# Optimization experiments

Hardware: AMD Instinct MI355X
Metric: run time of the kernel (lower is better)

The kernel has to match this reference:

```python
import jax, jax.numpy as jnp
import numpy as np

# Original torch code does the CZT in float64/complex128 explicitly; match it.
jax.config.update("jax_enable_x64", True)

SR = 44100
HOP = 512
MAX_NHAR = 128
REL_WIN = 4
F0_MIN = 40.0  # reconstruction of get_n_fft(): lowest analyzable pitch
N_MAX = int(round(SR / F0_MIN * REL_WIN / 2) * 2)          # 4410: max window size
N_FFT = int(2 ** np.ceil(np.log2(N_MAX)))                  # 8192: used only for padding
L = int(2 ** np.ceil(np.log2(N_MAX + MAX_NHAR - 1)))       # 8192: Bluestein conv length (exact for all frames since L >= n_i + m_i - 1)
N_FRAMES = 1024


def setup_inputs() -> dict:
    key = jax.random.key(0)
    k1, k2 = jax.random.split(key)
    t = N_FRAMES * HOP
    x = jax.random.normal(k1, (t,), dtype=jnp.float32)
    # pitch contour in a realistic 100..400 Hz voice range
    f0 = 100.0 + 300.0 * jax.random.uniform(k2, (N_FRAMES,), dtype=jnp.float32)
    return {"x": x, "f0": f0}


def _sinusoidal_analysis_czt(x, f0):
    # f0: (F,). Vectorized, padded/masked version of the per-frame CZT loop.
    f0 = jnp.clip(f0.astype(jnp.float64), F0_MIN, None)
    F = f0.shape[0]
    nhar = jnp.minimum(jnp.floor(SR / f0 / 2.0), float(MAX_NHAR)).astype(jnp.int32)      # (F,)
    winsize = (jnp.round(SR / f0 * REL_WIN / 2.0) * 2).astype(jnp.int32)                 # (F,) even, <= N_MAX
    pad = N_FFT // 2
    x_pad = jnp.pad(x.astype(jnp.float64), (pad, pad))

    j = jnp.arange(N_MAX)
    start = jnp.arange(F) * HOP + pad                                                    # (F,)
    idx = start[:, None] - winsize[:, None] // 2 + j[None, :]                            # (F, N_MAX)
    frames = x_pad[jnp.clip(idx, 0, x_pad.shape[0] - 1)]
    # torch.blackman_window(n) is periodic: denominator = n
    ratio = j[None, :].astype(jnp.float64) / winsize[:, None].astype(jnp.float64)
    win = 0.42 - 0.5 * jnp.cos(2.0 * np.pi * ratio) + 0.08 * jnp.cos(4.0 * np.pi * ratio)
    valid = j[None, :] < winsize[:, None]
    xw = jnp.where(valid, frames * win, 0.0)                                             # (F, N_MAX) windowed frame, zero-padded

    theta = 2.0 * np.pi * f0 / SR                                                        # (F,) A=exp(+i th), W=exp(-i th)
    jj = j.astype(jnp.float64)
    # gn[j] = x[j] * A^{-j} * W^{j^2/2} = x[j] * exp(-i th (j + j^2/2))
    gphase = -theta[:, None] * (jj[None, :] + 0.5 * jj[None, :] ** 2)
    gn = jnp.zeros((F, L), dtype=jnp.complex128).at[:, :N_MAX].set(xw * jnp.exp(1j * gphase))
    # hn[k] = 1/w[k] = exp(+i th k^2/2) for k < m ; hn[L-j] = exp(+i th j^2/2) for 1 <= j < n
    # (filled for the max ranges; extra entries are never reached because gn is zero beyond winsize)
    kk = jnp.arange(L)
    off = jnp.where(kk < MAX_NHAR, kk, jnp.where(kk > L - N_MAX, L - kk, 0)).astype(jnp.float64)
    hmask = (kk < MAX_NHAR) | (kk > L - N_MAX)
    hn = jnp.where(hmask[None, :], jnp.exp(1j * theta[:, None] * 0.5 * off[None, :] ** 2), 0.0 + 0.0j)
    qn = jnp.fft.ifft(jnp.fft.fft(gn, axis=-1) * jnp.fft.fft(hn, axis=-1), axis=-1)      # (F, L)

    m = jnp.arange(MAX_NHAR).astype(jnp.float64)
    wq = jnp.exp(-1j * theta[:, None] * 0.5 * m[None, :] ** 2)                           # w[:m]
    yn = qn[:, :MAX_NHAR] * wq                                                           # (F, MAX_NHAR)
    yn = 2.381 * yn / (winsize[:, None] // 2 + 1).astype(jnp.float64)
    har_mask = m[None, :] < nhar[:, None].astype(jnp.float64)
    ampl = jnp.where(har_mask, jnp.abs(yn), 0.0).T.astype(jnp.float32)                   # (MAX_NHAR, F)
    phase = jnp.where(har_mask, jnp.angle(yn), 0.0).T.astype(jnp.float32)
    return ampl, phase


def reference(x, f0):
    return _sinusoidal_analysis_czt(x, f0)
```

## Files before the change

kernel.cpp:

```cpp
#include <hip/hip_runtime.h>

#define HOP 512
#define MAX_NHAR 128
#define N_MAX 4410
#define ROWP 4416
#define SEGS 8
#define PI_D 3.14159265358979323846

__device__ __forceinline__ void frame_params(double f0v, int& w, int& nhar, double& theta) {
    double f0d = f0v < 40.0 ? 40.0 : f0v;
    const double inv = 44100.0 / f0d;
    nhar = (int)fmin(floor(inv * 0.5), 128.0);
    w = 2 * (int)rint(inv * 2.0);
    if (w > N_MAX) w = N_MAX;
    theta = (2.0 * PI_D * f0d) / 44100.0;
}

__device__ __forceinline__ int chunk8_of(int w) {
    return (((w + SEGS - 1) / SEGS) + 7) & ~7;
}

__global__ __launch_bounds__(128) void prep_kernel(
    const float* __restrict__ x, const float* __restrict__ f0,
    double* __restrict__ ccos, double* __restrict__ xw, int t, int F)
{
    const int f = blockIdx.x, tid = threadIdx.x;
    int w, nhar; double theta;
    frame_params((double)f0[f], w, nhar, theta);
    ccos[f * MAX_NHAR + tid] = cos(theta * (double)(tid + 1));

    const double invw = 1.0 / (double)w;
    double sa, ca, ss, cs;
    sincos((2.0 * PI_D) * ((double)tid * invw), &sa, &ca);
    sincos((2.0 * PI_D) * (128.0 * invw), &ss, &cs);
    double zr = ca, zi = sa;
    const int base = f * HOP - (w >> 1);
    double* row = xw + (size_t)f * ROWP;
    for (int j = tid; j < ROWP; j += 128) {
        double outv = 0.0;
        if (j < w) {
            const int ix = base + j;
            const double val = (ix >= 0 && ix < t) ? (double)x[ix] : 0.0;
            const double c = zr;
            const double win = 0.42 - 0.5 * c + 0.08 * (2.0 * c * c - 1.0);
            outv = val * win;
        }
        row[j] = outv;
        const double nzr = zr * cs - zi * ss;
        zi = zr * ss + zi * cs;
        zr = nzr;
    }
}

__global__ __launch_bounds__(64) void goertzel_kernel(
    const float* __restrict__ f0, const double* __restrict__ ccos,
    const double* __restrict__ xw, double2* __restrict__ parts, int F)
{
    const int frame = blockIdx.x >> 3;
    const int seg   = blockIdx.x & (SEGS - 1);
    const int lane  = threadIdx.x;

    int w, nhar; double theta;
    frame_params((double)f0[frame], w, nhar, theta);
    const int chunk = chunk8_of(w);
    const int j0 = seg * chunk;
    int lenp = 0;
    if (j0 < w) {
        const int l = w - j0;
        lenp = (l > chunk) ? chunk : ((l + 7) & ~7);
    }

    const double Ca = 2.0 * ccos[frame * MAX_NHAR + lane];
    const double Cb = 2.0 * ccos[frame * MAX_NHAR + lane + 64];
    double s1a = 0.0, s2a = 0.0, s1b = 0.0, s2b = 0.0;
    const double* __restrict__ row = xw + (size_t)frame * ROWP + j0;

    if (nhar > 64) {
        for (int jb = 0; jb < lenp; jb += 8) {
            double xv[8];
            #pragma unroll
            for (int u = 0; u < 8; ++u) xv[u] = row[jb + u];
            #pragma unroll
            for (int u = 0; u < 8; ++u) {
                const double ta = xv[u] - s2a;
                const double tb = xv[u] - s2b;
                const double na = fma(Ca, s1a, ta);
                const double nb = fma(Cb, s1b, tb);
                s2a = s1a; s1a = na;
                s2b = s1b; s1b = nb;
            }
        }
    } else {
        for (int jb = 0; jb < lenp; jb += 8) {
            double xv[8];
            #pragma unroll
            for (int u = 0; u < 8; ++u) xv[u] = row[jb + u];
            #pragma unroll
            for (int u = 0; u < 8; ++u) {
                const double ta = xv[u] - s2a;
                const double na = fma(Ca, s1a, ta);
                s2a = s1a; s1a = na;
            }
        }
    }
    double2* p = parts + (size_t)(frame * SEGS + seg) * MAX_NHAR;
    p[lane]      = make_double2(s1a, s2a);
    p[lane + 64] = make_double2(s1b, s2b);
}

__global__ __launch_bounds__(128) void finalize_kernel(
    const float* __restrict__ f0, const double2* __restrict__ parts,
    float* __restrict__ out, int F)
{
    const int frame = blockIdx.x;
    const int tid = threadIdx.x;

    int w, nhar; double theta;
    frame_params((double)f0[frame], w, nhar, theta);
    const int chunk = chunk8_of(w);
    const int slast = (w - 1) / chunk;
    const int endlast = slast * chunk + (((w - slast * chunk) + 7) & ~7);
    const double omega = theta * (double)(tid + 1);

    double sw, cw; sincos(omega, &sw, &cw);
    double sq, cq; sincos(omega * (double)chunk, &sq, &cq);
    double sl, cl; sincos(omega * (double)(endlast - 1), &sl, &cl);

    double Rr = cq * cw + sq * sw, Ri = cq * sw - sq * cw;
    double yr = 0.0, yi = 0.0;
    const double2* p = parts + (size_t)frame * SEGS * MAX_NHAR + tid;
    #pragma unroll
    for (int s = 0; s < SEGS; ++s) {
        const double2 v = p[(size_t)s * MAX_NHAR];
        const double tr = fma(-cw, v.y, v.x);
        const double ti = sw * v.y;
        const double Pr = (s == slast) ? cl : Rr;
        const double Pi = (s == slast) ? -sl : Ri;
        yr = fma(Pr, tr, fma(-Pi, ti, yr));
        yi = fma(Pr, ti, fma( Pi, tr, yi));
        const double nr = Rr * cq + Ri * sq;
        Ri = Ri * cq - Rr * sq; Rr = nr;
    }
    const double scale = 2.381 / (double)((w >> 1) + 1);
    yr *= scale; yi *= scale;

    float ampl = 0.0f, ph = 0.0f;
    if (tid < nhar) {
        ampl = (float)sqrt(yr * yr + yi * yi);
        ph   = (float)atan2(yi, yr);
    }
    out[tid * F + frame] = ampl;
    out[MAX_NHAR * F + tid * F + frame] = ph;
}

__global__ __launch_bounds__(128) void czt_direct_kernel(
    const float* __restrict__ x, const float* __restrict__ f0,
    float* __restrict__ out, int t, int F)
{
    __shared__ double sm[N_MAX];
    const int frame = blockIdx.x;
    const int tid = threadIdx.x;
    int w, nhar; double theta;
    frame_params((double)f0[frame], w, nhar, theta);
    {
        const double invw = 1.0 / (double)w;
        double sa, ca, ss, cs;
        sincos((2.0 * PI_D) * ((double)tid * invw), &sa, &ca);
        sincos((2.0 * PI_D) * (128.0 * invw), &ss, &cs);
        double zr = ca, zi = sa;
        const int base = frame * HOP - (w >> 1);
        for (int j = tid; j < w; j += 128) {
            const int ix = base + j;
            const double val = (ix >= 0 && ix < t) ? (double)x[ix] : 0.0;
            const double c = zr;
            const double win = 0.42 - 0.5 * c + 0.08 * (2.0 * c * c - 1.0);
            sm[j] = val * win;
            const double nzr = zr * cs - zi * ss;
            zi = zr * ss + zi * cs;
            zr = nzr;
        }
    }
    __syncthreads();
    double s, c;
    sincos(theta * (double)(tid + 1), &s, &c);
    const double rr = c, ri = -s;
    const double r2r = rr * rr - ri * ri, r2i = 2.0 * rr * ri;
    const double r4r = r2r * r2r - r2i * r2i, r4i = 2.0 * r2r * r2i;
    const double r3r = r2r * rr - r2i * ri, r3i = r2r * ri + r2i * rr;
    double z0r = 1.0, z0i = 0.0, z1r = rr, z1i = ri;
    double z2r = r2r, z2i = r2i, z3r = r3r, z3i = r3i;
    double a0r = 0, a0i = 0, a1r = 0, a1i = 0, a2r = 0, a2i = 0, a3r = 0, a3i = 0;
    const int w4 = w & ~3;
    for (int j = 0; j < w4; j += 4) {
        const double s0 = sm[j], s1 = sm[j + 1], s2 = sm[j + 2], s3 = sm[j + 3];
        double tr;
        a0r = fma(s0, z0r, a0r); a0i = fma(s0, z0i, a0i);
        tr = z0r * r4r - z0i * r4i; z0i = z0r * r4i + z0i * r4r; z0r = tr;
        a1r = fma(s1, z1r, a1r); a1i = fma(s1, z1i, a1i);
        tr = z1r * r4r - z1i * r4i; z1i = z1r * r4i + z1i * r4r; z1r = tr;
        a2r = fma(s2, z2r, a2r); a2i = fma(s2, z2i, a2i);
        tr = z2r * r4r - z2i * r4i; z2i = z2r * r4i + z2i * r4r; z2r = tr;
        a3r = fma(s3, z3r, a3r); a3i = fma(s3, z3i, a3i);
        tr = z3r * r4r - z3i * r4i; z3i = z3r * r4i + z3i * r4r; z3r = tr;
    }
    if (w4 < w) {
        const double s0 = sm[w4], s1 = sm[w4 + 1];
        a0r = fma(s0, z0r, a0r); a0i = fma(s0, z0i, a0i);
        a1r = fma(s1, z1r, a1r); a1i = fma(s1, z1i, a1i);
    }
    double yr = (a0r + a1r) + (a2r + a3r);
    double yi = (a0i + a1i) + (a2i + a3i);
    const double scale = 2.381 / (double)((w >> 1) + 1);
    yr *= scale; yi *= scale;
    float ampl = 0.0f, ph = 0.0f;
    if (tid < nhar) {
        ampl = (float)sqrt(yr * yr + yi * yi);
        ph   = (float)atan2(yi, yr);
    }
    out[tid * F + frame] = ampl;
    out[MAX_NHAR * F + tid * F + frame] = ph;
}

extern "C" void kernel_launch(void* const* d_in, const int* in_sizes, int n_in,
                              void* d_out, int out_size, void* d_ws, size_t ws_size,
                              hipStream_t stream) {
    const float* x  = (const float*)d_in[0];
    const float* f0 = (const float*)d_in[1];
    float* out = (float*)d_out;
    const int t = in_sizes[0];
    const int F = in_sizes[1];

    const size_t ccos_b  = (size_t)F * MAX_NHAR * sizeof(double);
    const size_t xw_b    = (size_t)F * ROWP * sizeof(double);
    const size_t parts_b = (size_t)F * SEGS * MAX_NHAR * sizeof(double2);
    if (ws_size >= ccos_b + xw_b + parts_b) {
        double*  ccos  = (double*)d_ws;
        double*  xw    = (double*)((char*)d_ws + ccos_b);
        double2* parts = (double2*)((char*)d_ws + ccos_b + xw_b);
        prep_kernel<<<F, 128, 0, stream>>>(x, f0, ccos, xw, t, F);
        goertzel_kernel<<<F * SEGS, 64, 0, stream>>>(f0, ccos, xw, parts, F);
        finalize_kernel<<<F, 128, 0, stream>>>(f0, parts, out, F);
    } else {
        czt_direct_kernel<<<F, 128, 0, stream>>>(x, f0, out, t, F);
    }
}
```

Baseline: 92.04 us.

## Fuse windowing into Goertzel kernel via shared memory, drop global xw buffer

Moves the Blackman-windowed frame construction from the prep kernel into the Goertzel kernel, with each block computing its own segment into shared memory. This removes writing and re-reading a ~36 MB double-precision windowed-frame buffer in global memory. In exchange, each element's window cosine is now computed with a direct cos call rather than a rotation recurrence, and the Goertzel loop reads from LDS. Sample reads become broadcasts from LDS instead of global loads.

Result: faster. 83.12 us (-9.7%).

```diff
diff --git a/kernel.cpp b/kernel.cpp
--- a/kernel.cpp
+++ b/kernel.cpp
@@ -3,8 +3,8 @@
 #define HOP 512
 #define MAX_NHAR 128
 #define N_MAX 4410
-#define ROWP 4416
 #define SEGS 8
+#define CHUNK_MAX 552
 #define PI_D 3.14159265358979323846
 
 __device__ __forceinline__ void frame_params(double f0v, int& w, int& nhar, double& theta) {
@@ -21,41 +21,20 @@
 }
 
 __global__ __launch_bounds__(128) void prep_kernel(
+    const float* __restrict__ f0, double* __restrict__ ccos, int F)
+{
+    const int f = blockIdx.x, k = threadIdx.x;
+    int w, nhar; double theta;
+    frame_params((double)f0[f], w, nhar, theta);
+    ccos[f * MAX_NHAR + k] = cos(theta * (double)(k + 1));
+}
+
+__global__ __launch_bounds__(64) void goertzel_kernel(
     const float* __restrict__ x, const float* __restrict__ f0,
-    double* __restrict__ ccos, double* __restrict__ xw, int t, int F)
-{
-    const int f = blockIdx.x, tid = threadIdx.x;
-    int w, nhar; double theta;
-    frame_params((double)f0[f], w, nhar, theta);
-    ccos[f * MAX_NHAR + tid] = cos(theta * (double)(tid + 1));
-
-    const double invw = 1.0 / (double)w;
-    double sa, ca, ss, cs;
-    sincos((2.0 * PI_D) * ((double)tid * invw), &sa, &ca);
-    sincos((2.0 * PI_D) * (128.0 * invw), &ss, &cs);
-    double zr = ca, zi = sa;
-    const int base = f * HOP - (w >> 1);
-    double* row = xw + (size_t)f * ROWP;
-    for (int j = tid; j < ROWP; j += 128) {
-        double outv = 0.0;
-        if (j < w) {
-            const int ix = base + j;
-            const double val = (ix >= 0 && ix < t) ? (double)x[ix] : 0.0;
-            const double c = zr;
-            const double win = 0.42 - 0.5 * c + 0.08 * (2.0 * c * c - 1.0);
-            outv = val * win;
-        }
-        row[j] = outv;
-        const double nzr = zr * cs - zi * ss;
-        zi = zr * ss + zi * cs;
-        zr = nzr;
-    }
-}
-
-__global__ __launch_bounds__(64) void goertzel_kernel(
-    const float* __restrict__ f0, const double* __restrict__ ccos,
-    const double* __restrict__ xw, double2* __restrict__ parts, int F)
-{
+    const double* __restrict__ ccos, double2* __restrict__ parts,
+    int t, int F)
+{
+    __shared__ double sm[CHUNK_MAX];
     const int frame = blockIdx.x >> 3;
     const int seg   = blockIdx.x & (SEGS - 1);
     const int lane  = threadIdx.x;
@@ -70,16 +49,32 @@
         lenp = (l > chunk) ? chunk : ((l + 7) & ~7);
     }
 
+    {
+        const double c2pi_invw = (2.0 * PI_D) / (double)w;
+        const int base = frame * HOP - (w >> 1) + j0;
+        for (int j = lane; j < lenp; j += 64) {
+            double outv = 0.0;
+            if (j0 + j < w) {
+                const int ix = base + j;
+                const double val = (ix >= 0 && ix < t) ? (double)x[ix] : 0.0;
+                const double c1 = cos(c2pi_invw * (double)(j0 + j));
+                const double win = fma(0.16, c1 * c1, 0.34) - 0.5 * c1;
+                outv = val * win;
+            }
+            sm[j] = outv;
+        }
+    }
+    __syncthreads();
+
     const double Ca = 2.0 * ccos[frame * MAX_NHAR + lane];
     const double Cb = 2.0 * ccos[frame * MAX_NHAR + lane + 64];
     double s1a = 0.0, s2a = 0.0, s1b = 0.0, s2b = 0.0;
-    const double* __restrict__ row = xw + (size_t)frame * ROWP + j0;
 
     if (nhar > 64) {
         for (int jb = 0; jb < lenp; jb += 8) {
             double xv[8];
             #pragma unroll
-            for (int u = 0; u < 8; ++u) xv[u] = row[jb + u];
+            for (int u = 0; u < 8; ++u) xv[u] = sm[jb + u];
             #pragma unroll
             for (int u = 0; u < 8; ++u) {
                 const double ta = xv[u] - s2a;
@@ -94,7 +89,7 @@
         for (int jb = 0; jb < lenp; jb += 8) {
             double xv[8];
             #pragma unroll
-            for (int u = 0; u < 8; ++u) xv[u] = row[jb + u];
+            for (int u = 0; u < 8; ++u) xv[u] = sm[jb + u];
             #pragma unroll
             for (int u = 0; u < 8; ++u) {
                 const double ta = xv[u] - s2a;
@@ -231,14 +226,12 @@
     const int F = in_sizes[1];
 
     const size_t ccos_b  = (size_t)F * MAX_NHAR * sizeof(double);
-    const size_t xw_b    = (size_t)F * ROWP * sizeof(double);
     const size_t parts_b = (size_t)F * SEGS * MAX_NHAR * sizeof(double2);
-    if (ws_size >= ccos_b + xw_b + parts_b) {
+    if (ws_size >= ccos_b + parts_b) {
         double*  ccos  = (double*)d_ws;
-        double*  xw    = (double*)((char*)d_ws + ccos_b);
-        double2* parts = (double2*)((char*)d_ws + ccos_b + xw_b);
-        prep_kernel<<<F, 128, 0, stream>>>(x, f0, ccos, xw, t, F);
-        goertzel_kernel<<<F * SEGS, 64, 0, stream>>>(f0, ccos, xw, parts, F);
+        double2* parts = (double2*)((char*)d_ws + ccos_b);
+        prep_kernel<<<F, 128, 0, stream>>>(f0, ccos, F);
+        goertzel_kernel<<<F * SEGS, 64, 0, stream>>>(x, f0, ccos, parts, t, F);
         finalize_kernel<<<F, 128, 0, stream>>>(f0, parts, out, F);
     } else {
         czt_direct_kernel<<<F, 128, 0, stream>>>(x, f0, out, t, F);
```
